# Kernel tuning notes

Measured on AMD Instinct MI355X. Metric: run time of the kernel, lower is better.

## Reference

```python
import jax, jax.numpy as jnp
import numpy as np

INPUT_SIZE = 784
HIDDEN = 512
NUM_CLASSES = 10
BATCH = 65536


def _linear_params(key, fan_in, fan_out):
    # torch nn.Linear default init: U(-1/sqrt(fan_in), 1/sqrt(fan_in))
    kw, kb = jax.random.split(key)
    bound = 1.0 / np.sqrt(fan_in)
    W = jax.random.uniform(kw, (fan_in, fan_out), jnp.float32, -bound, bound)
    b = jax.random.uniform(kb, (fan_out,), jnp.float32, -bound, bound)
    return W, b


def setup_inputs() -> dict:
    key = jax.random.key(0)
    keys = jax.random.split(key, 9)
    inp = {"x": jax.random.normal(keys[0], (BATCH, INPUT_SIZE), jnp.float32)}
    dims = [(INPUT_SIZE, HIDDEN)] + [(HIDDEN, HIDDEN)] * 6 + [(HIDDEN, NUM_CLASSES)]
    for i, (fi, fo) in enumerate(dims):
        W, b = _linear_params(keys[i + 1], fi, fo)
        inp[f"W{i + 1}"] = W
        inp[f"b{i + 1}"] = b
    return inp


def _dropout(x, p, key):
    # torch F.dropout (training=True): inverted dropout, keep prob = 1-p
    keep = jax.random.bernoulli(key, 1.0 - p, x.shape)
    return jnp.where(keep, x / (1.0 - p), 0.0).astype(x.dtype)


def reference(x, W1, b1, W2, b2, W3, b3, W4, b4, W5, b5, W6, b6, W7, b7, W8, b8):
    dk = jax.random.split(jax.random.key(42), 3)
    h = jax.nn.relu(x @ W1 + b1)                       # h1 + relu
    h = jax.nn.relu(_dropout(h @ W2 + b2, 0.2, dk[0])) # h2 + dropout(0.2) + relu
    h = jax.nn.relu(h @ W3 + b3)                       # h3 + relu
    h = jax.nn.relu(_dropout(h @ W4 + b4, 0.3, dk[1])) # h4 + dropout(0.3) + relu
    h = jax.nn.relu(h @ W5 + b5)                       # h5 + relu
    h = jax.nn.relu(_dropout(h @ W6 + b6, 0.5, dk[2])) # h6 + dropout(0.5) + relu
    h = jax.nn.relu(h @ W7 + b7)                       # h7 + relu
    logits = h @ W8 + b8                               # h8
    return jax.nn.softmax(logits, axis=-1)
```

## Files before the change

### kernel.cpp

```cpp
#include <hip/hip_runtime.h>
#include <cstdint>

#define ROTL32(v,n) (((v) << (n)) | ((v) >> (32 - (n))))

__host__ __forceinline__ void tf2x32(uint32_t k0, uint32_t k1,
                                     uint32_t x0, uint32_t x1,
                                     uint32_t& o0, uint32_t& o1)
{
  uint32_t k2 = k0 ^ k1 ^ 0x1BD11BDAu;
  x0 += k0; x1 += k1;
#define TF_RND(r) { x0 += x1; x1 = ROTL32(x1, (r)); x1 ^= x0; }
  TF_RND(13) TF_RND(15) TF_RND(26) TF_RND(6)
  x0 += k1; x1 += k2 + 1u;
  TF_RND(17) TF_RND(29) TF_RND(16) TF_RND(24)
  x0 += k2; x1 += k0 + 2u;
  TF_RND(13) TF_RND(15) TF_RND(26) TF_RND(6)
  x0 += k0; x1 += k1 + 3u;
  TF_RND(17) TF_RND(29) TF_RND(16) TF_RND(24)
  x0 += k1; x1 += k2 + 4u;
  TF_RND(13) TF_RND(15) TF_RND(26) TF_RND(6)
  x0 += k2; x1 += k0 + 5u;
#undef TF_RND
  o0 = x0; o1 = x1;
}

__device__ __forceinline__ void tf2x32_d(uint32_t k0, uint32_t k1,
                                         uint32_t x0, uint32_t x1,
                                         uint32_t& o0, uint32_t& o1)
{
  uint32_t k2 = k0 ^ k1 ^ 0x1BD11BDAu;
  x0 += k0; x1 += k1;
#define R_(r) { x0 += x1; x1 = __builtin_rotateleft32(x1, (r)); x1 ^= x0; }
  R_(13) R_(15) R_(26) R_(6)
  x0 += k1; x1 += k2 + 1u;
  R_(17) R_(29) R_(16) R_(24)
  x0 += k2; x1 += k0 + 2u;
  R_(13) R_(15) R_(26) R_(6)
  x0 += k0; x1 += k1 + 3u;
  R_(17) R_(29) R_(16) R_(24)
  x0 += k1; x1 += k2 + 4u;
  R_(13) R_(15) R_(26) R_(6)
  x0 += k2; x1 += k0 + 5u;
#undef R_
  o0 = x0; o1 = x1;
}

typedef __attribute__((ext_vector_type(8))) _Float16 h16x8;
typedef __attribute__((ext_vector_type(4))) float fl32x4;
typedef __attribute__((ext_vector_type(2))) unsigned long long u64x2;

__device__ __forceinline__ float u2unit_f(uint32_t b) {
  uint32_t r = (b >> 9) | 0x3F800000u;
  float f; __builtin_memcpy(&f, &r, 4); return f - 1.0f;
}

#define GLD16(gp, lp) \
  __builtin_amdgcn_global_load_lds( \
      (__attribute__((address_space(1))) void*)(gp), \
      (__attribute__((address_space(3))) void*)(lp), 16, 0, 0)

#define VMW(n) asm volatile("s_waitcnt vmcnt(" #n ")" ::: "memory")
#define LKW0() asm volatile("s_waitcnt lgkmcnt(0)" ::: "memory")
#define SBAR() asm volatile("s_barrier" ::: "memory")

__global__ __launch_bounds__(256) void cvt_x_f(const float* __restrict__ x,
                                               _Float16* __restrict__ xp,
                                               unsigned long long* __restrict__ m0,
                                               uint32_t k0, uint32_t k1)
{
  int idx = blockIdx.x * 256 + threadIdx.x;
  int row = idx / 104, c = idx - row * 104;
  h16x8 o = {0,0,0,0,0,0,0,0};
  if (c < 98) {
    const fl32x4* p = (const fl32x4*)&x[row * 784 + c * 8];
    fl32x4 a = p[0], b = p[1];
    o[0] = (_Float16)a[0]; o[1] = (_Float16)a[1]; o[2] = (_Float16)a[2]; o[3] = (_Float16)a[3];
    o[4] = (_Float16)b[0]; o[5] = (_Float16)b[1]; o[6] = (_Float16)b[2]; o[7] = (_Float16)b[3];
  }
  *(h16x8*)&xp[row * 832 + c * 8] = o;

  uint32_t lane = threadIdx.x & 63u;
  uint32_t gw = (uint32_t)blockIdx.x * 4u + ((uint32_t)threadIdx.x >> 6);
#pragma unroll
  for (int i = 0; i < 3; ++i) {
    uint32_t wix = gw * 3u + (uint32_t)i;
    uint32_t b1, b2;
    tf2x32_d(k0, k1, 0u, wix * 64u + lane, b1, b2);
    unsigned long long mw = __ballot(u2unit_f(b1 ^ b2) < 0.8f);
    if (lane == 0) m0[wix] = mw;
  }
}

__global__ __launch_bounds__(256) void cvt_w_f(
    const float* __restrict__ W1, const float* __restrict__ W2, const float* __restrict__ W3,
    const float* __restrict__ W4, const float* __restrict__ W5, const float* __restrict__ W6,
    const float* __restrict__ W7, _Float16* __restrict__ WT1, _Float16* __restrict__ WT,
    unsigned long long* __restrict__ m0, uint32_t k0, uint32_t k1)
{
  int b = blockIdx.x;
  if (b < 1666) {
    int idx = b * 256 + threadIdx.x;
    int n = idx / 832, k = idx - n * 832;
    WT1[idx] = (k < 784) ? (_Float16)W1[k * 512 + n] : (_Float16)0.f;
  } else {
    int l = (b - 1666) >> 10;
    int idx = ((b - 1666) & 1023) * 256 + threadIdx.x;
    int n = idx >> 9, k = idx & 511;
    const float* Wp = (l == 0) ? W2 : (l == 1) ? W3 : (l == 2) ? W4
                    : (l == 3) ? W5 : (l == 4) ? W6 : W7;
    WT[l * 262144 + idx] = (_Float16)Wp[k * 512 + n];
  }
  uint32_t lane = threadIdx.x & 63u;
  uint32_t gw = (uint32_t)blockIdx.x * 4u + ((uint32_t)threadIdx.x >> 6);
#pragma unroll
  for (int i = 0; i < 7; ++i) {
    uint32_t wix = 319488u + gw * 7u + (uint32_t)i;
    if (wix < 524288u) {
      uint32_t b1, b2;
      tf2x32_d(k0, k1, 0u, wix * 64u + lane, b1, b2);
      unsigned long long mw = __ballot(u2unit_f(b1 ^ b2) < 0.8f);
      if (lane == 0) m0[wix] = mw;
    }
  }
}

template<bool DROP, bool HEAD>
__global__ __launch_bounds__(256, 4) void gemm_r(
    const _Float16* __restrict__ A, const _Float16* __restrict__ BT,
    const float* __restrict__ bias, const unsigned long long* __restrict__ mask,
    float invq, _Float16* __restrict__ C, int K,
    unsigned long long* __restrict__ mout, uint32_t mbase, int tfcap,
    uint32_t mk0, uint32_t mk1, float mq,
    const float* __restrict__ W8g, float* __restrict__ plog)
{
  __shared__ __align__(16) _Float16 sm[16384];
  const int tid  = threadIdx.x;
  const int lane = tid & 63;
  const int wv   = tid >> 6;
  const int wr   = wv >> 1, wc = wv & 1;
  const int rml  = lane & 15;
  const int kq   = lane >> 4;

  int bid = blockIdx.x;
  int t = (bid & 7) * 256 + (bid >> 3);
  int bm = (t >> 2) * 128;
  int bn = (t & 3) * 128;

  const int sp   = tid >> 3;
  const int sin  = (tid & 7) ^ (sp & 7);
  const int srow = 2 * sp + (sin >> 2);
  const int sk16 = sin & 3;

  const _Float16* pA0 = A  + (size_t)(bm + srow)      * K + sk16 * 8;
  const _Float16* pA1 = A  + (size_t)(bm + srow + 64) * K + sk16 * 8;
  const _Float16* pB0 = BT + (size_t)(bn + srow)      * K + sk16 * 8;
  const _Float16* pB1 = BT + (size_t)(bn + srow + 64) * K + sk16 * 8;

  const int rslot = (((rml & 1) << 2) | kq) ^ (rml >> 1);
  const int abase = (wr * 32 + (rml >> 1)) * 64 + rslot * 8;
  const int bbase = 4096 + (wc * 32 + (rml >> 1)) * 64 + rslot * 8;

  fl32x4 acc[4][4];
#pragma unroll
  for (int i = 0; i < 4; ++i)
#pragma unroll
    for (int j = 0; j < 4; ++j)
      acc[i][j] = (fl32x4){0.f, 0.f, 0.f, 0.f};

  const int nst = K >> 5;
  const int nd  = nst >> 1;

#define STAGEP(selem) do {                                                     \
    GLD16(pA0, sm + (selem) + wv * 512);                                       \
    GLD16(pA1, sm + (selem) + 2048 + wv * 512);                                \
    GLD16(pB0, sm + (selem) + 4096 + wv * 512);                                \
    GLD16(pB1, sm + (selem) + 6144 + wv * 512);                                \
  } while (0)
#define ADVP() do { pA0 += 32; pA1 += 32; pB0 += 32; pB1 += 32; } while (0)

#define HOST2() do {                                                           \
    if (mout != nullptr && tfc < tfcap) {                                      \
      _Pragma("unroll")                                                        \
      for (int i_ = 0; i_ < 2; ++i_) {                                         \
        uint32_t a_, b_;                                                       \
        tf2x32_d(mk0, mk1, 0u, xrun, a_, b_);                                  \
        unsigned long long bal = __ballot(u2unit_f(a_ ^ b_) < mq);             \
        if (lane == tfc) mw0 = bal;                                            \
        ++tfc; xrun += 64u;                                                    \
      }                                                                        \
    } } while (0)

#define COMPUTE(selem) do {                                                    \
    h16x8 af[4], bf[4];                                                        \
    _Pragma("unroll")                                                          \
    for (int mf = 0; mf < 4; ++mf)                                             \
      af[mf] = *(const h16x8*)&sm[(selem) + abase + mf * 512];                 \
    _Pragma("unroll")                                                          \
    for (int nf = 0; nf < 4; ++nf)                                             \
      bf[nf] = *(const h16x8*)&sm[(selem) + bbase + nf * 512];                 \
    _Pragma("unroll")                                                          \
    for (int mf = 0; mf < 4; ++mf)                                             \
      _Pragma("unroll")                                                        \
      for (int nf = 0; nf < 4; ++nf)                                           \
        acc[mf][nf] = __builtin_amdgcn_mfma_f32_16x16x32_f16(                  \
            af[mf], bf[nf], acc[mf][nf], 0, 0, 0);                             \
  } while (0)

  STAGEP(0);
  ADVP();

  uint64_t mw0 = 0;
  int tfc = 0;
  uint32_t gw = (uint32_t)bid * 4u + (uint32_t)wv;
  uint32_t xrun = (mbase + gw * (uint32_t)tfcap) * 64u + (uint32_t)lane;

#pragma unroll 1
  for (int it = 0; it < nd - 1; ++it) {
    STAGEP(8192); ADVP();
    HOST2();
    VMW(4); SBAR();
    COMPUTE(0);
    SBAR();
    STAGEP(0); ADVP();
    HOST2();
    VMW(4); SBAR();
    COMPUTE(8192);
    SBAR();
  }
  STAGEP(8192);
  HOST2();
  VMW(4); SBAR();
  COMPUTE(0);
  SBAR();
  HOST2();
  VMW(0); SBAR();
  COMPUTE(8192);
  SBAR();
#undef STAGEP
#undef ADVP
#undef HOST2
#undef COMPUTE

  if (mout != nullptr && lane < tfcap)
    mout[mbase + gw * (uint32_t)tfcap + (uint32_t)lane] = mw0;

  const int eb = wv * 2176;
  const int lrr = lane >> 1;

  if (HEAD) {
    float* W8l = (float*)(sm + 9216);
    for (int i = tid; i < 1280; i += 256) {
      int k = i / 10, c = i - k * 10;
      W8l[i] = W8g[(size_t)(bn + k) * 10 + c];
    }
    __syncthreads();
    float* pout = plog + (size_t)((t & 3) * 2 + wc) * 655360;
    const int ch = lane & 1;

#define HEPI(HALF) do {                                                        \
    _Pragma("unroll")                                                          \
    for (int nf = 0; nf < 4; ++nf) {                                           \
      int colq = nf * 16 + rml;                                                \
      float bv = bias[bn + wc * 64 + colq];                                    \
      _Pragma("unroll")                                                        \
      for (int mfh = 0; mfh < 2; ++mfh) {                                      \
        _Pragma("unroll")                                                      \
        for (int r = 0; r < 4; ++r) {                                          \
          int lr = mfh * 16 + kq * 4 + r;                                      \
          float v = fmaxf(acc[(HALF) * 2 + mfh][nf][r] + bv, 0.0f);            \
          sm[eb + lr * 68 + colq] = (_Float16)v;                               \
        }                                                                      \
      }                                                                        \
    }                                                                          \
    LKW0();                                                                    \
    {                                                                          \
      float p[10];                                                             \
      _Pragma("unroll")                                                        \
      for (int c = 0; c < 10; ++c) p[c] = 0.f;                                 \
      _Pragma("unroll")                                                        \
      for (int j = 0; j < 4; ++j) {                                            \
        h16x8 hv = *(const h16x8*)&sm[eb + lrr * 68 + ch * 32 + j * 8];        \
        _Pragma("unroll")                                                      \
        for (int e = 0; e < 8; ++e) {                                          \
          float hf = (float)hv[e];                                             \
          const float* wrow = &W8l[(wc * 64 + ch * 32 + j * 8 + e) * 10];      \
          _Pragma("unroll")                                                    \
          for (int c = 0; c < 10; ++c) p[c] += hf * wrow[c];                   \
        }                                                                      \
      }                                                                        \
      _Pragma("unroll")                                                        \
      for (int c = 0; c < 10; ++c) p[c] += __shfl_xor(p[c], 1);                \
      if (ch == 0) {                                                           \
        int row = bm + wr * 64 + (HALF) * 32 + lrr;                            \
        _Pragma("unroll")                                                      \
        for (int c = 0; c < 10; ++c) pout[(size_t)row * 10 + c] = p[c];        \
      }                                                                        \
    }                                                                          \
  } while (0)

    HEPI(0);
    HEPI(1);
#undef HEPI
    return;
  }

  const int cbase = (lane & 1) * 4;

#define EPIHALF(HALF) do {                                                     \
    _Pragma("unroll")                                                          \
    for (int nf = 0; nf < 4; ++nf) {                                           \
      int colq = nf * 16 + rml;                                                \
      float bv = bias[bn + wc * 64 + colq];                                    \
      _Pragma("unroll")                                                        \
      for (int mfh = 0; mfh < 2; ++mfh) {                                      \
        _Pragma("unroll")                                                      \
        for (int r = 0; r < 4; ++r) {                                          \
          int lr = mfh * 16 + kq * 4 + r;                                      \
          float v = fmaxf(acc[(HALF) * 2 + mfh][nf][r] + bv, 0.0f) * invq;     \
          sm[eb + lr * 68 + colq] = (_Float16)v;                               \
        }                                                                      \
      }                                                                        \
    }                                                                          \
    LKW0();                                                                    \
    {                                                                          \
      int grow = bm + wr * 64 + (HALF) * 32 + lrr;                             \
      int col0 = bn + wc * 64;                                                 \
      uint64_t mw = 0;                                                         \
      if (DROP) mw = mask[(size_t)grow * 8 + (size_t)(col0 >> 6)];             \
      _Pragma("unroll")                                                        \
      for (int c = 0; c < 4; ++c) {                                            \
        int cc = cbase + c;                                                    \
        uint64_t lo = *(const uint64_t*)&sm[eb + lrr * 68 + cc * 8];           \
        uint64_t hi = *(const uint64_t*)&sm[eb + lrr * 68 + cc * 8 + 4];       \
        if (DROP) {                                                            \
          uint32_t bits = (uint32_t)(mw >> (cc * 8)) & 0xffu;                  \
          uint64_t klo = 0, khi = 0;                                           \
          if (bits & 0x01u) klo |= 0x000000000000ffffull;                      \
          if (bits & 0x02u) klo |= 0x00000000ffff0000ull;                      \
          if (bits & 0x04u) klo |= 0x0000ffff00000000ull;                      \
          if (bits & 0x08u) klo |= 0xffff000000000000ull;                      \
          if (bits & 0x10u) khi |= 0x000000000000ffffull;                      \
          if (bits & 0x20u) khi |= 0x00000000ffff0000ull;                      \
          if (bits & 0x40u) khi |= 0x0000ffff00000000ull;                      \
          if (bits & 0x80u) khi |= 0xffff000000000000ull;                      \
          lo &= klo; hi &= khi;                                                \
        }                                                                      \
        u64x2 ov; ov[0] = lo; ov[1] = hi;                                      \
        *(u64x2*)&C[(size_t)grow * 512 + col0 + cc * 8] = ov;                  \
      }                                                                        \
    }                                                                          \
  } while (0)

  EPIHALF(0);
  EPIHALF(1);
#undef EPIHALF
}

__global__ __launch_bounds__(256) void smax_k(const float* __restrict__ plog,
                                              const float* __restrict__ b8,
                                              float* __restrict__ out)
{
  int row = blockIdx.x * 256 + threadIdx.x;
  float l[10];
#pragma unroll
  for (int c = 0; c < 10; ++c) l[c] = b8[c];
#pragma unroll
  for (int s = 0; s < 8; ++s) {
    const float* pr = &plog[(size_t)s * 655360 + (size_t)row * 10];
#pragma unroll
    for (int c = 0; c < 10; ++c) l[c] += pr[c];
  }
  float mx = l[0];
#pragma unroll
  for (int c = 1; c < 10; ++c) mx = fmaxf(mx, l[c]);
  float sum = 0.f, e[10];
#pragma unroll
  for (int c = 0; c < 10; ++c) { e[c] = expf(l[c] - mx); sum += e[c]; }
  float is = 1.0f / sum;
#pragma unroll
  for (int c = 0; c < 10; ++c) out[(size_t)row * 10 + c] = e[c] * is;
}

extern "C" void kernel_launch(void* const* d_in, const int* in_sizes, int n_in,
                              void* d_out, int out_size, void* d_ws, size_t ws_size,
                              hipStream_t stream) {
  (void)in_sizes; (void)n_in; (void)out_size; (void)ws_size;
  const float* x = (const float*)d_in[0];
  const float* W[8]; const float* B[8];
  for (int i = 0; i < 8; ++i) { W[i] = (const float*)d_in[1 + 2*i]; B[i] = (const float*)d_in[2 + 2*i]; }

  char* w = (char*)d_ws;
  _Float16* xpad = (_Float16*)(w);
  float*    plog = (float*)(w);
  _Float16* hA   = (_Float16*)(w + 109051904);
  _Float16* hB   = (_Float16*)(w + 176160768);
  _Float16* WT1  = (_Float16*)(w + 243269632);
  _Float16* WT   = (_Float16*)(w + 244121600);
  unsigned long long* masks = (unsigned long long*)(w + 247267328);
  unsigned long long* mL0 = masks;
  unsigned long long* mL1 = masks + 524288;
  unsigned long long* mL2 = masks + 1048576;

  uint32_t d00,d01,d10,d11,d20,d21;
  tf2x32(0u, 42u, 0u, 0u, d00, d01);
  tf2x32(0u, 42u, 0u, 1u, d10, d11);
  tf2x32(0u, 42u, 0u, 2u, d20, d21);

  cvt_x_f<<<26624, 256, 0, stream>>>(x, xpad, mL0, d00, d01);
  cvt_w_f<<<7810, 256, 0, stream>>>(W[0],W[1],W[2],W[3],W[4],W[5],W[6], WT1, WT,
                                    mL0, d00, d01);

  dim3 g(2048), b(256);
  gemm_r<false,false><<<g, b, 0, stream>>>(xpad, WT1,           B[0], nullptr, 1.0f,      hA, 832,
                                     nullptr, 0u, 0, 0u, 0u, 0.f, nullptr, nullptr);
  gemm_r<true ,false><<<g, b, 0, stream>>>(hA,   WT + 0*262144, B[1], mL0,     1.0f/0.8f, hB, 512,
                                     mL1, 0u,       32, d10, d11, 0.7f, nullptr, nullptr);
  gemm_r<false,false><<<g, b, 0, stream>>>(hB,   WT + 1*262144, B[2], nullptr, 1.0f,      hA, 512,
                                     mL1, 262144u,  32, d10, d11, 0.7f, nullptr, nullptr);
  gemm_r<true ,false><<<g, b, 0, stream>>>(hA,   WT + 2*262144, B[3], mL1,     1.0f/0.7f, hB, 512,
                                     mL2, 0u,       32, d20, d21, 0.5f, nullptr, nullptr);
  gemm_r<false,false><<<g, b, 0, stream>>>(hB,   WT + 3*262144, B[4], nullptr, 1.0f,      hA, 512,
                                     mL2, 262144u,  32, d20, d21, 0.5f, nullptr, nullptr);
  gemm_r<true ,false><<<g, b, 0, stream>>>(hA,   WT + 4*262144, B[5], mL2,     2.0f,      hB, 512,
                                     nullptr, 0u, 0, 0u, 0u, 0.f, nullptr, nullptr);
  gemm_r<false,true ><<<g, b, 0, stream>>>(hB,   WT + 5*262144, B[6], nullptr, 1.0f,      hA, 512,
                                     nullptr, 0u, 0, 0u, 0u, 0.f, W[7], plog);
  smax_k<<<256, 256, 0, stream>>>(plog, B[7], (float*)d_out);
}
```

Measured before the change: 549.4 us.

## Fuse fp32-to-fp16 input conversion into first GEMM and move dropout mask generation

Removes the separate input conversion kernel and adds a dedicated first-layer GEMM that loads fp32 x tiles straight into LDS and converts them to fp16 while building MFMA fragments. Layer-0 dropout mask generation moves into this GEMM, interleaved with the K loop, and cvt_w_f now covers the rest of the mask range. This avoids writing and re-reading a padded fp16 copy of x and saves a launch. In exchange the first GEMM stages twice as many bytes per A tile through LDS, needs a larger LDS footprint (occupancy bound lowered to 3), and needs special handling of the ragged K tail at 784.

```diff
diff --git a/kernel.cpp b/kernel.cpp
--- a/kernel.cpp
+++ b/kernel.cpp
@@ -63,34 +63,6 @@
 #define LKW0() asm volatile("s_waitcnt lgkmcnt(0)" ::: "memory")
 #define SBAR() asm volatile("s_barrier" ::: "memory")
 
-__global__ __launch_bounds__(256) void cvt_x_f(const float* __restrict__ x,
-                                               _Float16* __restrict__ xp,
-                                               unsigned long long* __restrict__ m0,
-                                               uint32_t k0, uint32_t k1)
-{
-  int idx = blockIdx.x * 256 + threadIdx.x;
-  int row = idx / 104, c = idx - row * 104;
-  h16x8 o = {0,0,0,0,0,0,0,0};
-  if (c < 98) {
-    const fl32x4* p = (const fl32x4*)&x[row * 784 + c * 8];
-    fl32x4 a = p[0], b = p[1];
-    o[0] = (_Float16)a[0]; o[1] = (_Float16)a[1]; o[2] = (_Float16)a[2]; o[3] = (_Float16)a[3];
-    o[4] = (_Float16)b[0]; o[5] = (_Float16)b[1]; o[6] = (_Float16)b[2]; o[7] = (_Float16)b[3];
-  }
-  *(h16x8*)&xp[row * 832 + c * 8] = o;
-
-  uint32_t lane = threadIdx.x & 63u;
-  uint32_t gw = (uint32_t)blockIdx.x * 4u + ((uint32_t)threadIdx.x >> 6);
-#pragma unroll
-  for (int i = 0; i < 3; ++i) {
-    uint32_t wix = gw * 3u + (uint32_t)i;
-    uint32_t b1, b2;
-    tf2x32_d(k0, k1, 0u, wix * 64u + lane, b1, b2);
-    unsigned long long mw = __ballot(u2unit_f(b1 ^ b2) < 0.8f);
-    if (lane == 0) m0[wix] = mw;
-  }
-}
-
 __global__ __launch_bounds__(256) void cvt_w_f(
     const float* __restrict__ W1, const float* __restrict__ W2, const float* __restrict__ W3,
     const float* __restrict__ W4, const float* __restrict__ W5, const float* __restrict__ W6,
@@ -113,8 +85,8 @@
   uint32_t lane = threadIdx.x & 63u;
   uint32_t gw = (uint32_t)blockIdx.x * 4u + ((uint32_t)threadIdx.x >> 6);
 #pragma unroll
-  for (int i = 0; i < 7; ++i) {
-    uint32_t wix = 319488u + gw * 7u + (uint32_t)i;
+  for (int i = 0; i < 9; ++i) {
+    uint32_t wix = 262144u + gw * 9u + (uint32_t)i;
     if (wix < 524288u) {
       uint32_t b1, b2;
       tf2x32_d(k0, k1, 0u, wix * 64u + lane, b1, b2);
@@ -122,6 +94,191 @@
       if (lane == 0) m0[wix] = mw;
     }
   }
+}
+
+__global__ __launch_bounds__(256, 3) void gemm_x1(
+    const float* __restrict__ X, const _Float16* __restrict__ BT,
+    const float* __restrict__ bias, _Float16* __restrict__ C,
+    unsigned long long* __restrict__ mout,
+    uint32_t mk0, uint32_t mk1, float mq)
+{
+  __shared__ __align__(16) _Float16 sm[24576];
+  const int tid  = threadIdx.x;
+  const int lane = tid & 63;
+  const int wv   = tid >> 6;
+  const int wr   = wv >> 1, wc = wv & 1;
+  const int rml  = lane & 15;
+  const int kq   = lane >> 4;
+
+  int bid = blockIdx.x;
+  int t = (bid & 7) * 256 + (bid >> 3);
+  int bm = (t >> 2) * 128;
+  int bn = (t & 3) * 128;
+
+  const int tr8 = tid >> 3;
+  const int sc  = (tid & 7) ^ (tr8 & 7);
+  const float* bX0 = X + (size_t)(bm + tr8) * 784;
+  const float* bX1 = X + (size_t)(bm + 32 + tr8) * 784;
+  const float* bX2 = X + (size_t)(bm + 64 + tr8) * 784;
+  const float* bX3 = X + (size_t)(bm + 96 + tr8) * 784;
+  const float* pX0 = bX0 + sc * 4;
+  const float* pX1 = bX1 + sc * 4;
+  const float* pX2 = bX2 + sc * 4;
+  const float* pX3 = bX3 + sc * 4;
+
+  const int sp   = tid >> 3;
+  const int sin  = (tid & 7) ^ (sp & 7);
+  const int srow = 2 * sp + (sin >> 2);
+  const int sk16 = sin & 3;
+  const _Float16* pB0 = BT + (size_t)(bn + srow)      * 832 + sk16 * 8;
+  const _Float16* pB1 = BT + (size_t)(bn + srow + 64) * 832 + sk16 * 8;
+
+  const int rslot = (((rml & 1) << 2) | kq) ^ (rml >> 1);
+  const int bbase = 8192 + (wc * 32 + (rml >> 1)) * 64 + rslot * 8;
+
+  fl32x4 acc[4][4];
+#pragma unroll
+  for (int i = 0; i < 4; ++i)
+#pragma unroll
+    for (int j = 0; j < 4; ++j)
+      acc[i][j] = (fl32x4){0.f, 0.f, 0.f, 0.f};
+
+#define STAGEX(selem) do {                                                     \
+    GLD16(pX0, sm + (selem) + wv * 512);                                       \
+    GLD16(pX1, sm + (selem) + 2048 + wv * 512);                                \
+    GLD16(pX2, sm + (selem) + 4096 + wv * 512);                                \
+    GLD16(pX3, sm + (selem) + 6144 + wv * 512);                                \
+    GLD16(pB0, sm + (selem) + 8192 + wv * 512);                                \
+    GLD16(pB1, sm + (selem) + 10240 + wv * 512);                               \
+  } while (0)
+#define ADVX() do { pX0 += 32; pX1 += 32; pX2 += 32; pX3 += 32;                \
+                    pB0 += 32; pB1 += 32; } while (0)
+
+#define HOST2() do {                                                           \
+    if (tfc < 32) {                                                            \
+      _Pragma("unroll")                                                        \
+      for (int i_ = 0; i_ < 2; ++i_) {                                         \
+        uint32_t a_, b_;                                                       \
+        tf2x32_d(mk0, mk1, 0u, xrun, a_, b_);                                  \
+        unsigned long long bal = __ballot(u2unit_f(a_ ^ b_) < mq);             \
+        if (lane == tfc) mw0 = bal;                                            \
+        ++tfc; xrun += 64u;                                                    \
+      }                                                                        \
+    } } while (0)
+
+#define COMPUTEX(selem) do {                                                   \
+    h16x8 af[4], bf[4];                                                        \
+    _Pragma("unroll")                                                          \
+    for (int mf = 0; mf < 4; ++mf) {                                           \
+      int row_ = wr * 64 + mf * 16 + rml;                                      \
+      int c0_ = (2 * kq) ^ (rml & 7);                                          \
+      fl32x4 lo = *(const fl32x4*)&sm[(selem) + row_ * 64 + c0_ * 8];          \
+      fl32x4 hi = *(const fl32x4*)&sm[(selem) + row_ * 64 + (c0_ ^ 1) * 8];    \
+      af[mf][0] = (_Float16)lo[0]; af[mf][1] = (_Float16)lo[1];                \
+      af[mf][2] = (_Float16)lo[2]; af[mf][3] = (_Float16)lo[3];                \
+      af[mf][4] = (_Float16)hi[0]; af[mf][5] = (_Float16)hi[1];                \
+      af[mf][6] = (_Float16)hi[2]; af[mf][7] = (_Float16)hi[3];                \
+    }                                                                          \
+    _Pragma("unroll")                                                          \
+    for (int nf = 0; nf < 4; ++nf)                                             \
+      bf[nf] = *(const h16x8*)&sm[(selem) + bbase + nf * 512];                 \
+    _Pragma("unroll")                                                          \
+    for (int mf = 0; mf < 4; ++mf)                                             \
+      _Pragma("unroll")                                                        \
+      for (int nf = 0; nf < 4; ++nf)                                           \
+        acc[mf][nf] = __builtin_amdgcn_mfma_f32_16x16x32_f16(                  \
+            af[mf], bf[nf], acc[mf][nf], 0, 0, 0);                             \
+  } while (0)
+
+  STAGEX(0);
+  ADVX();
+
+  uint64_t mw0 = 0;
+  int tfc = 0;
+  uint32_t gw = (uint32_t)bid * 4u + (uint32_t)wv;
+  uint32_t xrun = (gw * 32u) * 64u + (uint32_t)lane;
+
+#pragma unroll 1
+  for (int kt = 0; kt < 23; ++kt) {
+    const int scur = (kt & 1) * 12288;
+    STAGEX(12288 - scur); ADVX();
+    HOST2();
+    VMW(6); SBAR();
+    COMPUTEX(scur);
+    SBAR();
+  }
+  {
+    GLD16((sc <= 3) ? pX0 : bX0, sm + 0 + wv * 512);
+    GLD16((sc <= 3) ? pX1 : bX1, sm + 2048 + wv * 512);
+    GLD16((sc <= 3) ? pX2 : bX2, sm + 4096 + wv * 512);
+    GLD16((sc <= 3) ? pX3 : bX3, sm + 6144 + wv * 512);
+    GLD16(pB0, sm + 8192 + wv * 512);
+    GLD16(pB1, sm + 10240 + wv * 512);
+    pB0 += 32; pB1 += 32;
+  }
+  HOST2();
+  VMW(6); SBAR();
+  COMPUTEX(12288);
+  SBAR();
+  {
+    GLD16(bX0, sm + 12288 + wv * 512);
+    GLD16(bX1, sm + 12288 + 2048 + wv * 512);
+    GLD16(bX2, sm + 12288 + 4096 + wv * 512);
+    GLD16(bX3, sm + 12288 + 6144 + wv * 512);
+    GLD16(pB0, sm + 12288 + 8192 + wv * 512);
+    GLD16(pB1, sm + 12288 + 10240 + wv * 512);
+  }
+  HOST2();
+  VMW(6); SBAR();
+  COMPUTEX(0);
+  SBAR();
+  VMW(0); SBAR();
+  COMPUTEX(12288);
+  SBAR();
+#undef STAGEX
+#undef ADVX
+#undef HOST2
+#undef COMPUTEX
+
+  if (lane < 32) mout[gw * 32u + (uint32_t)lane] = mw0;
+
+  const int eb = wv * 2176;
+  const int lrr = lane >> 1;
+  const int cbase = (lane & 1) * 4;
+
+#define EPIHALF(HALF) do {                                                     \
+    _Pragma("unroll")                                                          \
+    for (int nf = 0; nf < 4; ++nf) {                                           \
+      int colq = nf * 16 + rml;                                                \
+      float bv = bias[bn + wc * 64 + colq];                                    \
+      _Pragma("unroll")                                                        \
+      for (int mfh = 0; mfh < 2; ++mfh) {                                      \
+        _Pragma("unroll")                                                      \
+        for (int r = 0; r < 4; ++r) {                                          \
+          int lr = mfh * 16 + kq * 4 + r;                                      \
+          float v = fmaxf(acc[(HALF) * 2 + mfh][nf][r] + bv, 0.0f);            \
+          sm[eb + lr * 68 + colq] = (_Float16)v;                               \
+        }                                                                      \
+      }                                                                        \
+    }                                                                          \
+    LKW0();                                                                    \
+    {                                                                          \
+      int grow = bm + wr * 64 + (HALF) * 32 + lrr;                             \
+      int col0 = bn + wc * 64;                                                 \
+      _Pragma("unroll")                                                        \
+      for (int c = 0; c < 4; ++c) {                                            \
+        int cc = cbase + c;                                                    \
+        uint64_t lo = *(const uint64_t*)&sm[eb + lrr * 68 + cc * 8];           \
+        uint64_t hi = *(const uint64_t*)&sm[eb + lrr * 68 + cc * 8 + 4];       \
+        u64x2 ov; ov[0] = lo; ov[1] = hi;                                      \
+        *(u64x2*)&C[(size_t)grow * 512 + col0 + cc * 8] = ov;                  \
+      }                                                                        \
+    }                                                                          \
+  } while (0)
+
+  EPIHALF(0);
+  EPIHALF(1);
+#undef EPIHALF
 }
 
 template<bool DROP, bool HEAD>
@@ -390,7 +547,6 @@
   for (int i = 0; i < 8; ++i) { W[i] = (const float*)d_in[1 + 2*i]; B[i] = (const float*)d_in[2 + 2*i]; }
 
   char* w = (char*)d_ws;
-  _Float16* xpad = (_Float16*)(w);
   float*    plog = (float*)(w);
   _Float16* hA   = (_Float16*)(w + 109051904);
   _Float16* hB   = (_Float16*)(w + 176160768);
@@ -406,13 +562,11 @@
   tf2x32(0u, 42u, 0u, 1u, d10, d11);
   tf2x32(0u, 42u, 0u, 2u, d20, d21);
 
-  cvt_x_f<<<26624, 256, 0, stream>>>(x, xpad, mL0, d00, d01);
   cvt_w_f<<<7810, 256, 0, stream>>>(W[0],W[1],W[2],W[3],W[4],W[5],W[6], WT1, WT,
                                     mL0, d00, d01);
 
   dim3 g(2048), b(256);
-  gemm_r<false,false><<<g, b, 0, stream>>>(xpad, WT1,           B[0], nullptr, 1.0f,      hA, 832,
-                                     nullptr, 0u, 0, 0u, 0u, 0.f, nullptr, nullptr);
+  gemm_x1<<<g, b, 0, stream>>>(x, WT1, B[0], hA, mL0, d00, d01, 0.8f);
   gemm_r<true ,false><<<g, b, 0, stream>>>(hA,   WT + 0*262144, B[1], mL0,     1.0f/0.8f, hB, 512,
                                      mL1, 0u,       32, d10, d11, 0.7f, nullptr, nullptr);
   gemm_r<false,false><<<g, b, 0, stream>>>(hB,   WT + 1*262144, B[2], nullptr, 1.0f,      hA, 512,
```

Measured after the change: 555.8 us. About the same (+1.2%).
